# Kernel optimization log

Hardware: AMD Instinct MI355X
Metric: run time of the kernel (lower is better)

## Reference

```python
import jax, jax.numpy as jnp
import numpy as np

N = 8192   # num_nodes
H = 128    # hidden_dim
B = 100    # batch of events
K = 5      # num_neg_samples
TD_MAX = 10000.0
TIME_SD = jnp.array([50.0, 7.0, 15.0, 15.0])  # time_sd from forward; time_mean = 0


def setup_inputs() -> dict:
    key = jax.random.key(0)
    ks = jax.random.split(key, 16)
    p = 32.0 / N  # avg degree ~32
    A = (jax.random.uniform(ks[0], (N, N)) < p).astype(jnp.float32)
    # S init: S[v,u] = 1/D[v] for neighbors u (row-normalized A)
    S = A / (A.sum(axis=1, keepdims=True) + 1e-7)
    z0 = jax.random.normal(ks[1], (N, H)) * 0.1
    u = jax.random.randint(ks[2], (B,), 0, N)
    v = jax.random.randint(ks[3], (B,), 0, N)
    event_types = jax.random.randint(ks[4], (B,), 0, 2)
    neg_idx = jax.random.randint(ks[5], (B, 2 * K), 0, N)
    time_diff = jax.random.normal(ks[6], (B, 2, 4))
    t_bar = jax.random.uniform(ks[7], (B, N)) * 1000.0
    t = 1000.0 + 10.0 * jnp.arange(B, dtype=jnp.float32)

    def lin(k, o, i):
        k1, k2 = jax.random.split(k)
        lim = 1.0 / np.sqrt(i)
        return (jax.random.uniform(k1, (o, i), minval=-lim, maxval=lim),
                jax.random.uniform(k2, (o,), minval=-lim, maxval=lim))

    om0_w, om0_b = lin(ks[8], 1, 2 * H)
    om1_w, om1_b = lin(ks[9], 1, 2 * H)
    Wh_w, Wh_b = lin(ks[10], H, H)
    Ws_w, Ws_b = lin(ks[11], H, H)
    Wr_w, Wr_b = lin(ks[12], H, H)
    Wt_w, Wt_b = lin(ks[13], H, 4)
    return dict(u=u, v=v, event_types=event_types, neg_idx=neg_idx,
                time_diff=time_diff, t_bar=t_bar, t=t, z0=z0, A=A, S=S,
                w_t=0.5 * jnp.ones(2), alpha=0.5 * jnp.ones(2), psi=0.5 * jnp.ones(2),
                om0_w=om0_w, om0_b=om0_b, om1_w=om1_w, om1_b=om1_b,
                Wh_w=Wh_w, Wh_b=Wh_b, Ws_w=Ws_w, Ws_b=Ws_b,
                Wr_w=Wr_w, Wr_b=Wr_b, Wt_w=Wt_w, Wt_b=Wt_b)


def _forward(u, v, event_types, neg_idx, time_diff, t_bar, t, z0, A, S,
             w_t, alpha, psi, om0_w, om0_b, om1_w, om1_b,
             Wh_w, Wh_b, Ws_w, Ws_b, Wr_w, Wr_b, Wt_w, Wt_b):
    td_norm = time_diff / TIME_SD  # (td - 0) / sd

    def hawkes(zu, zv, et, td):
        # lambda = psi * log(1 + exp(g/psi)) + alpha * exp(-w_t * td/td_max)
        zc = jnp.concatenate([zu, zv], axis=-1)
        g0 = jnp.einsum('...d,d->...', zc, om0_w[0]) + om0_b[0]
        g1 = jnp.einsum('...d,d->...', zc, om1_w[0]) + om1_b[0]
        g = jnp.where(et == 0, g0, g1)
        ps, al, wt = psi[et], alpha[et], w_t[et]
        gp = jnp.clip(g / (ps + 1e-7), -75.0, 75.0)
        return ps * jnp.log1p(jnp.exp(gp)) + al * jnp.exp(-wt * (td / TD_MAX))

    ar = jnp.arange(N)

    def step(z, ev):
        u_it, v_it, et, td2, tb, t_it, neg = ev
        z_u, z_v = z[u_it], z[v_it]
        Wh_all = z @ Wh_w.T + Wh_b  # [N,H]

        def struct(node):
            # structural attention over node's neighbors (masked, not dense loop)
            mask = A[node] > 0
            q = jnp.exp(S[node]) * mask
            q = q / (q.sum() + 1e-7)
            hsig = jax.nn.sigmoid(q[:, None] * Wh_all)
            hmax = jnp.where(mask[:, None], hsig, -jnp.inf).max(axis=0)
            return jnp.where(jnp.any(mask), hmax, 0.0)

        # update of u uses struct info from v's neighborhood, and vice versa
        hs = jnp.stack([struct(v_it), struct(u_it)])  # [2,H]
        h = (hs @ Ws_w.T + Ws_b) + (jnp.stack([z_u, z_v]) @ Wr_w.T + Wr_b) + (td2 @ Wt_w.T + Wt_b)
        z_upd = jax.nn.sigmoid(h)
        z_new = z.at[u_it].set(z_upd[0]).at[v_it].set(z_upd[1])

        # negative pairs: (u, v_neg_k) then (u_neg_k, v), using z_prev
        v_neg, u_neg = neg[:K], neg[K:]
        zu_neg = jnp.concatenate([jnp.broadcast_to(z_u, (K, H)), z[u_neg]], 0)
        zv_neg = jnp.concatenate([z[v_neg], jnp.broadcast_to(z_v, (K, H))], 0)
        lt_u = jnp.concatenate([jnp.full((K,), tb[u_it]), tb[u_neg]])
        lt_v = jnp.concatenate([tb[v_neg], jnp.full((K,), tb[v_it])])
        ts_neg = t_it - jnp.maximum(lt_u, lt_v)
        ts_pos = t_it - jnp.maximum(tb[u_it], tb[v_it])

        # all-node intensity prediction (Lambda_dict path, detached in torch)
        zd = jax.lax.stop_gradient(z)
        zu_all = jnp.concatenate([jnp.broadcast_to(jax.lax.stop_gradient(z_u), (N, H)),
                                  jnp.broadcast_to(jax.lax.stop_gradient(z_v), (N, H))], 0)
        zv_all = jnp.concatenate([zd, zd], 0)
        last_t = jnp.maximum(
            jnp.concatenate([jnp.full((N,), tb[u_it]), jnp.full((N,), tb[v_it])]),
            jnp.concatenate([tb, tb]))
        lam_all = hawkes(zu_all, zv_all, jnp.full((2 * N,), et),
                         jax.lax.stop_gradient(t_it - last_t))
        m = ((ar != u_it) & (ar != v_it)).astype(lam_all.dtype)
        lam_sum = jax.lax.stop_gradient(jnp.sum(lam_all * jnp.concatenate([m, m])))

        return z_new, (z_u, z_v, zu_neg, zv_neg, ts_pos, ts_neg, lam_sum)

    _, (zu_p, zv_p, zun, zvn, ts_p, ts_n, lam_sums) = jax.lax.scan(
        step, z0, (u, v, event_types, td_norm, t_bar, t, neg_idx))

    lam_pos = hawkes(zu_p, zv_p, event_types, ts_p)            # [B]
    lam_neg = hawkes(zun, zvn, event_types[:, None], ts_n)      # [B,2K]
    return jnp.concatenate([lam_pos[:, None], lam_neg, lam_sums[:, None]], axis=1)  # [B, 2K+2]


def reference(u, v, event_types, neg_idx, time_diff, t_bar, t, z0, A, S,
              w_t, alpha, psi, om0_w, om0_b, om1_w, om1_b,
              Wh_w, Wh_b, Ws_w, Ws_b, Wr_w, Wr_b, Wt_w, Wt_b):
    return _forward(u, v, event_types, neg_idx, time_diff, t_bar, t, z0, A, S,
                    w_t, alpha, psi, om0_w, om0_b, om1_w, om1_b,
                    Wh_w, Wh_b, Ws_w, Ws_b, Wr_w, Wr_b, Wt_w, Wt_b)
```

## Files before the change

kernel.cpp:

```cpp
#include <hip/hip_runtime.h>
#include <math.h>

#define N 8192
#define H 128
#define BB 100
#define KK 5
#define MAXN 256
#define TD_MAXF 10000.0f

#define OFF_WHALLV ((size_t)N * H)
#define OFF_ZVER (OFF_WHALLV + 2 * BB * H)

__global__ __launch_bounds__(256) void prep_weights_kernel(
    const float* __restrict__ Wh, const float* __restrict__ Ws,
    const float* __restrict__ Wr, const float* __restrict__ om0,
    const float* __restrict__ om1, float* __restrict__ WhT,
    float* __restrict__ WsT, float* __restrict__ WrT, float* __restrict__ omP,
    unsigned* __restrict__ flags) {
  int idx = blockIdx.x * 256 + threadIdx.x;
  if (idx < H * H) {
    int d = idx >> 7, k = idx & (H - 1);
    WhT[k * H + d] = Wh[d * H + k];
  } else if (idx < 2 * H * H) {
    int e = idx - H * H;
    int d = e >> 7, k = e & (H - 1);
    WsT[k * H + d] = Ws[d * H + k];
  } else if (idx < 3 * H * H) {
    int e = idx - 2 * H * H;
    int d = e >> 7, k = e & (H - 1);
    WrT[k * H + d] = Wr[d * H + k];
  } else if (idx < 3 * H * H + 2 * H) {
    int e = idx - 3 * H * H;
    omP[e] = om0[e];
  } else if (idx < 3 * H * H + 4 * H) {
    int e = idx - 3 * H * H - 2 * H;
    omP[2 * H + e] = om1[e];
  } else if (idx < 3 * H * H + 4 * H + 4 * BB + 4) {
    int e = idx - (3 * H * H + 4 * H);
    flags[e] = 0u;
  }
}

__global__ __launch_bounds__(256) void dbase_kernel(
    const float* __restrict__ z0, const float* __restrict__ om0,
    const float* __restrict__ om1, float* __restrict__ dvec0) {
  int j = blockIdx.x * 256 + threadIdx.x;
  if (j >= N) return;
  const float4* zr = (const float4*)(z0 + (size_t)j * H);
  const float4* o0 = (const float4*)om0;
  const float4* o1 = (const float4*)om1;
  float a0 = 0, b0 = 0, a1 = 0, b1 = 0;
  for (int k = 0; k < H / 4; ++k) {
    float4 zv = zr[k];
    float4 l0 = o0[k], r0 = o0[k + H / 4];
    float4 l1 = o1[k], r1 = o1[k + H / 4];
    a0 += zv.x * l0.x + zv.y * l0.y + zv.z * l0.z + zv.w * l0.w;
    b0 += zv.x * r0.x + zv.y * r0.y + zv.z * r0.z + zv.w * r0.w;
    a1 += zv.x * l1.x + zv.y * l1.y + zv.z * l1.z + zv.w * l1.w;
    b1 += zv.x * r1.x + zv.y * r1.y + zv.z * r1.z + zv.w * r1.w;
  }
  dvec0[0 * N + j] = a0;
  dvec0[1 * N + j] = b0;
  dvec0[2 * N + j] = a1;
  dvec0[3 * N + j] = b1;
}

__global__ __launch_bounds__(128) void whall_kernel(
    const float* __restrict__ z0, const float* __restrict__ WhT,
    const float* __restrict__ Wh_b, float* __restrict__ whall) {
  int n = blockIdx.x;
  __shared__ float zr[H];
  zr[threadIdx.x] = z0[(size_t)n * H + threadIdx.x];
  __syncthreads();
  int d = threadIdx.x;
  float acc = Wh_b[d];
#pragma unroll 8
  for (int k = 0; k < H; ++k) acc += zr[k] * WhT[k * H + d];
  whall[(size_t)n * H + d] = acc;
}

__global__ __launch_bounds__(256) void nbr_kernel(
    const int* __restrict__ u, const int* __restrict__ v,
    const float* __restrict__ A, const float* __restrict__ S,
    int* __restrict__ cnt, int* __restrict__ nidx, float* __restrict__ nes,
    float* __restrict__ qsum) {
  int l = blockIdx.x;
  int b = l >> 1, r = l & 1;
  int node = r ? u[b] : v[b];
  const int tid = threadIdx.x;
  __shared__ int cnts[256];
  __shared__ int excl[257];
  __shared__ float ssum[256];
  int c = 0;
  float local = 0.0f;
  for (int it = 0; it < N / 256; ++it) {
    int j = it * 256 + tid;
    if (A[(size_t)node * N + j] > 0.0f) {
      ++c;
      local += expf(S[(size_t)node * N + j]);
    }
  }
  cnts[tid] = c;
  ssum[tid] = local;
  __syncthreads();
  if (tid == 0) {
    int s = 0;
    for (int i = 0; i < 256; ++i) { excl[i] = s; s += cnts[i]; }
    excl[256] = s;
  }
  __syncthreads();
  int p = excl[tid];
  for (int it = 0; it < N / 256; ++it) {
    int j = it * 256 + tid;
    if (A[(size_t)node * N + j] > 0.0f) {
      if (p < MAXN) {
        nidx[l * MAXN + p] = j;
        nes[l * MAXN + p] = expf(S[(size_t)node * N + j]);
      }
      ++p;
    }
  }
  __syncthreads();
  for (int s = 128; s > 0; s >>= 1) {
    if (tid < s) ssum[tid] += ssum[tid + s];
    __syncthreads();
  }
  if (tid == 0) {
    cnt[l] = min(excl[256], MAXN);
    qsum[l] = ssum[0];
  }
}

__global__ __launch_bounds__(256) void dag_prep_kernel(
    const int* __restrict__ u_, const int* __restrict__ v_,
    const int* __restrict__ cnt_, const int* __restrict__ nidx_,
    int* __restrict__ woff, int* __restrict__ zsrc, unsigned* __restrict__ need) {
  int l = blockIdx.x;
  int b = l >> 1, r = l & 1;
  const int tid = threadIdx.x;
  __shared__ int uL[BB], vL[BB];
  if (tid < BB) {
    uL[tid] = u_[tid];
    vL[tid] = v_[tid];
  }
  __syncthreads();
  int c = cnt_[l];
  for (int i = tid; i < c; i += 256) {
    int n = nidx_[l * MAXN + i];
    int a = -1, row = 0;
    for (int s = b - 1; s >= 0; --s) {
      if (vL[s] == n) { a = s; row = 1; break; }
      if (uL[s] == n) { a = s; row = 0; break; }
    }
    int off;
    if (a < 0) {
      off = n * H;
    } else {
      off = (int)OFF_WHALLV + (2 * a + row) * H;
      atomicOr(&need[b * 4 + (a >> 5)], 1u << (a & 31));
    }
    woff[l * MAXN + i] = off;
  }
  if (r == 0 && tid >= 254) {
    int which = tid - 254;
    int node = which ? vL[b] : uL[b];
    int a = -1, row = 0;
    for (int s = b - 1; s >= 0; --s) {
      if (vL[s] == node) { a = s; row = 1; break; }
      if (uL[s] == node) { a = s; row = 0; break; }
    }
    int sv = -1;
    if (a >= 0) {
      sv = 2 * a + row;
      atomicOr(&need[b * 4 + (a >> 5)], 1u << (a & 31));
    }
    zsrc[2 * b + which] = sv;
  }
}

__global__ __launch_bounds__(1024) void step_kernel(
    const int* __restrict__ u_, const int* __restrict__ v_,
    const float* __restrict__ time_diff, const float* __restrict__ z0,
    const float* __restrict__ WhT, const float* __restrict__ WsT,
    const float* __restrict__ WrT, const float* __restrict__ omP,
    const float* __restrict__ Wh_b, const float* __restrict__ Ws_b,
    const float* __restrict__ Wr_b, const float* __restrict__ Wt_w,
    const float* __restrict__ Wt_b, const float* __restrict__ wsf,
    float* __restrict__ zver, float* __restrict__ whallv,
    float* __restrict__ dlog, const float* __restrict__ qsum_,
    const int* __restrict__ cnt_, const float* __restrict__ nes_,
    const int* __restrict__ woff_, const int* __restrict__ zsrc_,
    const unsigned* __restrict__ need, unsigned* done) {
  const int b = blockIdx.x;
  const int t = threadIdx.x;
  __shared__ int woffS[2][MAXN];
  __shared__ float nqS[2][MAXN];
  __shared__ float scratch[8][2][H];
  __shared__ float hsS[2][H];
  __shared__ float zrowS[2][H];
  __shared__ float zupdS[2][H];
  __shared__ float td2S[2][4];
  __shared__ int cntS[2], zsrcS[2], uvS[2];
  __shared__ float invqS[2];

  if (t < 512) {
    int r = t >> 8, i = t & 255;
    int l = 2 * b + r;
    woffS[r][i] = woff_[l * MAXN + i];
    nqS[r][i] = nes_[l * MAXN + i];
  } else if (t < 520) {
    int i = t - 512;
    int c = i & 3;
    float sd = (c == 0) ? 50.0f : ((c == 1) ? 7.0f : 15.0f);
    td2S[i >> 2][c] = time_diff[b * 8 + i] / sd;
  } else if (t < 522) {
    int r = t - 520;
    cntS[r] = cnt_[2 * b + r];
    invqS[r] = 1.0f / (qsum_[2 * b + r] + 1e-7f);
    zsrcS[r] = zsrc_[2 * b + r];
  } else if (t == 522) {
    uvS[0] = u_[b];
  } else if (t == 523) {
    uvS[1] = v_[b];
  }
  if (t == 0) {
    for (int w = 0; w < 4; ++w) {
      unsigned nw = need[b * 4 + w];
      while ((atomicOr(&done[w], 0u) & nw) != nw) __builtin_amdgcn_s_sleep(1);
    }
    __threadfence();
  }
  __syncthreads();

  const int ub = uvS[0], vb = uvS[1];

  {
    int r = t >> 9;
    int sub = (t >> 7) & 3;
    int d = t & (H - 1);
    int c = cntS[r];
    float iq = invqS[r];
    float mx = -INFINITY;
#pragma unroll 4
    for (int i = sub; i < c; i += 4)
      mx = fmaxf(mx, nqS[r][i] * iq * wsf[(size_t)woffS[r][i] + d]);
    scratch[sub][r][d] = mx;
  }
  if (t < 256) {
    int r = t >> 7, d = t & (H - 1);
    int s = zsrcS[r];
    int node = r ? vb : ub;
    if (s < 0)
      zrowS[r][d] = z0[(size_t)node * H + d];
    else
      zrowS[r][d] = wsf[OFF_ZVER + (size_t)s * H + d];
  }
  __syncthreads();

  if (t < 2 * H) {
    int r = t >> 7, d = t & (H - 1);
    float m = fmaxf(fmaxf(scratch[0][r][d], scratch[1][r][d]),
                    fmaxf(scratch[2][r][d], scratch[3][r][d]));
    hsS[r][d] = (cntS[r] > 0) ? (1.0f / (1.0f + expf(-m))) : 0.0f;
  }
  __syncthreads();

  {
    int ks = t >> 7;
    int d = t & (H - 1);
    int k0 = ks * 16;
    float a0 = 0.0f, a1 = 0.0f;
#pragma unroll 4
    for (int k = k0; k < k0 + 16; ++k) {
      float ws = WsT[k * H + d], wr = WrT[k * H + d];
      a0 += hsS[0][k] * ws + zrowS[0][k] * wr;
      a1 += hsS[1][k] * ws + zrowS[1][k] * wr;
    }
    scratch[ks][0][d] = a0;
    scratch[ks][1][d] = a1;
  }
  __syncthreads();

  if (t < 2 * H) {
    int r = t >> 7, d = t & (H - 1);
    float acc = Ws_b[d] + Wr_b[d] + Wt_b[d];
#pragma unroll
    for (int ks = 0; ks < 8; ++ks) acc += scratch[ks][r][d];
    acc += td2S[r][0] * Wt_w[d * 4 + 0] + td2S[r][1] * Wt_w[d * 4 + 1] +
           td2S[r][2] * Wt_w[d * 4 + 2] + td2S[r][3] * Wt_w[d * 4 + 3];
    float zu = 1.0f / (1.0f + expf(-acc));
    zupdS[r][d] = zu;
    zver[(size_t)(2 * b + r) * H + d] = zu;
  }
  __syncthreads();

  {
    int ks = t >> 7;
    int d = t & (H - 1);
    int k0 = ks * 16;
    int r0 = (ub == vb) ? 1 : 0;
    float a0 = 0.0f, a1 = 0.0f;
#pragma unroll 4
    for (int k = k0; k < k0 + 16; ++k) {
      float wh = WhT[k * H + d];
      a0 += zupdS[r0][k] * wh;
      a1 += zupdS[1][k] * wh;
    }
    scratch[ks][0][d] = a0;
    scratch[ks][1][d] = a1;
  }
  __syncthreads();

  if (t < 2 * H) {
    int r = t >> 7, d = t & (H - 1);
    float acc = Wh_b[d];
#pragma unroll
    for (int ks = 0; ks < 8; ++ks) acc += scratch[ks][r][d];
    whallv[(size_t)(2 * b + r) * H + d] = acc;
  } else if (t < 768) {
    int w = (t - 256) >> 6;
    int lane = t & 63;
    int row = w >> 2;
    int which = w & 3;
    int rr = (row == 0 && ub == vb) ? 1 : row;
    int wsel = which >> 1;
    int off = (which & 1) * H;
    float val = zupdS[rr][lane] * omP[wsel * 2 * H + off + lane] +
                zupdS[rr][64 + lane] * omP[wsel * 2 * H + off + 64 + lane];
    for (int s = 32; s > 0; s >>= 1) val += __shfl_down(val, s);
    if (lane == 0) dlog[b * 8 + which * 2 + row] = val;
  }
  __syncthreads();

  if (t == 0) {
    __threadfence();
    atomicOr(&done[b >> 5], 1u << (b & 31));
  }
}

__global__ __launch_bounds__(256) void lam_kernel(
    const int* __restrict__ u, const int* __restrict__ v,
    const int* __restrict__ etypes, const int* __restrict__ neg_,
    const float* __restrict__ t_bar, const float* __restrict__ tt,
    const float* __restrict__ w_t, const float* __restrict__ alpha,
    const float* __restrict__ psi, const float* __restrict__ om0_b,
    const float* __restrict__ om1_b, const float* __restrict__ dvec0,
    const float* __restrict__ dlog, float* __restrict__ out) {
  const int b = blockIdx.x;
  const int tid = threadIdx.x;
  __shared__ float dR[N];
  __shared__ int uS[BB], vS[BB];
  __shared__ float red[256];
  __shared__ float suS, svS;

  const int e = etypes[b];
  const int ub = u[b], vb = v[b];
  const float ps = psi[e], al = alpha[e], wt = w_t[e];
  const float ob0 = om0_b[0], ob1 = om1_b[0];
  const float ob = e ? ob1 : ob0;
  const float tcur = tt[b];
  const float inv_ps = 1.0f / (ps + 1e-7f);
  const int whichR = 2 * e + 1;
  const int whichL = 2 * e;

  if (tid < BB) {
    uS[tid] = u[tid];
    vS[tid] = v[tid];
  }
  {
    const float4* base = (const float4*)(dvec0 + (size_t)whichR * N);
    float4* dst = (float4*)dR;
    for (int i = tid; i < N / 4; i += 256) dst[i] = base[i];
  }
  __syncthreads();

  for (int i = tid; i < b; i += 256) {
    int ui = uS[i], vi = vS[i];
    bool u_over = (ui == vi);
    bool v_over = false;
    for (int j = i + 1; j < b; ++j) {
      int uj = uS[j], vj = vS[j];
      u_over = u_over || (uj == ui) || (vj == ui);
      v_over = v_over || (uj == vi) || (vj == vi);
    }
    if (!u_over) dR[ui] = dlog[i * 8 + whichR * 2 + 0];
    if (!v_over) dR[vi] = dlog[i * 8 + whichR * 2 + 1];
  }

  if (tid < 13) {
    auto dpre = [&](int x, int which) -> float {
      for (int bp = b - 1; bp >= 0; --bp) {
        if (vS[bp] == x) return dlog[bp * 8 + which * 2 + 1];
        if (uS[bp] == x) return dlog[bp * 8 + which * 2 + 0];
      }
      return dvec0[(size_t)which * N + x];
    };
    if (tid < 11) {
      int li, ri;
      float ltu, ltv;
      if (tid == 0) {
        li = ub; ri = vb;
        ltu = t_bar[(size_t)b * N + ub];
        ltv = t_bar[(size_t)b * N + vb];
      } else if (tid <= 5) {
        int vn = neg_[b * (2 * KK) + (tid - 1)];
        li = ub; ri = vn;
        ltu = t_bar[(size_t)b * N + ub];
        ltv = t_bar[(size_t)b * N + vn];
      } else {
        int un = neg_[b * (2 * KK) + (tid - 1)];
        li = un; ri = vb;
        ltu = t_bar[(size_t)b * N + un];
        ltv = t_bar[(size_t)b * N + vb];
      }
      float g = dpre(li, whichL) + dpre(ri, whichR) + ob;
      float gp = fminf(fmaxf(g * inv_ps, -75.0f), 75.0f);
      float ts = tcur - fmaxf(ltu, ltv);
      out[b * 12 + tid] =
          ps * log1pf(expf(gp)) + al * expf(-wt * (ts / TD_MAXF));
    } else if (tid == 11) {
      suS = dpre(ub, whichL);
    } else {
      svS = dpre(vb, whichL);
    }
  }
  __syncthreads();

  const float su = suS, sv = svS;
  const float tb_u = t_bar[(size_t)b * N + ub];
  const float tb_v = t_bar[(size_t)b * N + vb];
  float acc = 0.0f;
  for (int j = tid; j < N; j += 256) {
    if (j == ub || j == vb) continue;
    float d = dR[j];
    float tbj = t_bar[(size_t)b * N + j];
    float gu = su + d + ob;
    float gv = sv + d + ob;
    float gpu_ = fminf(fmaxf(gu * inv_ps, -75.0f), 75.0f);
    float gpv_ = fminf(fmaxf(gv * inv_ps, -75.0f), 75.0f);
    float spl = ps * (log1pf(expf(gpu_)) + log1pf(expf(gpv_)));
    float tdu = tcur - fmaxf(tb_u, tbj);
    float tdv = tcur - fmaxf(tb_v, tbj);
    float ex = al * (expf(-wt * (tdu / TD_MAXF)) + expf(-wt * (tdv / TD_MAXF)));
    acc += spl + ex;
  }
  red[tid] = acc;
  __syncthreads();
  for (int s = 128; s > 0; s >>= 1) {
    if (tid < s) red[tid] += red[tid + s];
    __syncthreads();
  }
  if (tid == 0) out[b * 12 + 11] = red[0];
}

extern "C" void kernel_launch(void* const* d_in, const int* in_sizes, int n_in,
                              void* d_out, int out_size, void* d_ws,
                              size_t ws_size, hipStream_t stream) {
  const int* u = (const int*)d_in[0];
  const int* v = (const int*)d_in[1];
  const int* et = (const int*)d_in[2];
  const int* neg = (const int*)d_in[3];
  const float* time_diff = (const float*)d_in[4];
  const float* t_bar = (const float*)d_in[5];
  const float* t = (const float*)d_in[6];
  const float* z0 = (const float*)d_in[7];
  const float* A = (const float*)d_in[8];
  const float* S = (const float*)d_in[9];
  const float* w_t = (const float*)d_in[10];
  const float* alpha = (const float*)d_in[11];
  const float* psi = (const float*)d_in[12];
  const float* om0_w = (const float*)d_in[13];
  const float* om0_b = (const float*)d_in[14];
  const float* om1_w = (const float*)d_in[15];
  const float* om1_b = (const float*)d_in[16];
  const float* Wh_w = (const float*)d_in[17];
  const float* Wh_b = (const float*)d_in[18];
  const float* Ws_w = (const float*)d_in[19];
  const float* Ws_b = (const float*)d_in[20];
  const float* Wr_w = (const float*)d_in[21];
  const float* Wr_b = (const float*)d_in[22];
  const float* Wt_w = (const float*)d_in[23];
  const float* Wt_b = (const float*)d_in[24];
  float* out = (float*)d_out;

  float* wsf = (float*)d_ws;
  float* whall = wsf;
  float* whallv = wsf + OFF_WHALLV;
  float* zver = wsf + OFF_ZVER;
  float* WhT = zver + 2 * BB * H;
  float* WsT = WhT + H * H;
  float* WrT = WsT + H * H;
  float* omP = WrT + H * H;
  float* dvec0 = omP + 4 * H;
  float* dlog = dvec0 + 4 * N;
  float* qsum = dlog + 8 * BB;
  int* cnt = (int*)(qsum + 2 * BB);
  int* nidx = cnt + 2 * BB;
  float* nes = (float*)(nidx + 2 * BB * MAXN);
  int* woff = (int*)(nes + 2 * BB * MAXN);
  int* zsrc = woff + 2 * BB * MAXN;
  unsigned* need = (unsigned*)(zsrc + 2 * BB);
  unsigned* done = need + 4 * BB;

  prep_weights_kernel<<<(3 * H * H + 4 * H + 4 * BB + 4 + 255) / 256, 256, 0,
                        stream>>>(Wh_w, Ws_w, Wr_w, om0_w, om1_w, WhT, WsT,
                                  WrT, omP, need);
  dbase_kernel<<<(N + 255) / 256, 256, 0, stream>>>(z0, om0_w, om1_w, dvec0);
  whall_kernel<<<N, H, 0, stream>>>(z0, WhT, Wh_b, whall);
  nbr_kernel<<<2 * BB, 256, 0, stream>>>(u, v, A, S, cnt, nidx, nes, qsum);
  dag_prep_kernel<<<2 * BB, 256, 0, stream>>>(u, v, cnt, nidx, woff, zsrc,
                                              need);
  step_kernel<<<BB, 1024, 0, stream>>>(
      u, v, time_diff, z0, WhT, WsT, WrT, omP, Wh_b, Ws_b, Wr_b, Wt_w, Wt_b,
      wsf, zver, whallv, dlog, qsum, cnt, nes, woff, zsrc, need, done);
  lam_kernel<<<BB, 256, 0, stream>>>(u, v, et, neg, t_bar, t, w_t, alpha, psi,
                                     om0_b, om1_b, dvec0, dlog, out);
}
```

Baseline: 645.9 us.

## Merge prep kernels, prefetch independent neighbors before dependency wait, widen lam kernel

```diff
diff --git a/kernel.cpp b/kernel.cpp
--- a/kernel.cpp
+++ b/kernel.cpp
@@ -11,86 +11,89 @@
 #define OFF_WHALLV ((size_t)N * H)
 #define OFF_ZVER (OFF_WHALLV + 2 * BB * H)
 
-__global__ __launch_bounds__(256) void prep_weights_kernel(
+__global__ __launch_bounds__(256) void prep_all_kernel(
     const float* __restrict__ Wh, const float* __restrict__ Ws,
     const float* __restrict__ Wr, const float* __restrict__ om0,
-    const float* __restrict__ om1, float* __restrict__ WhT,
-    float* __restrict__ WsT, float* __restrict__ WrT, float* __restrict__ omP,
-    unsigned* __restrict__ flags) {
+    const float* __restrict__ om1, const float* __restrict__ z0,
+    float* __restrict__ WhT, float* __restrict__ WsT, float* __restrict__ WrT,
+    float* __restrict__ omP, unsigned* __restrict__ flags,
+    float* __restrict__ dvec0) {
+  const int B0 = H * H, B1 = 2 * H * H, B2 = 3 * H * H;
+  const int B3 = B2 + 2 * H, B4 = B2 + 4 * H, B5 = B4 + 4 * BB + 4;
   int idx = blockIdx.x * 256 + threadIdx.x;
-  if (idx < H * H) {
+  if (idx < B0) {
     int d = idx >> 7, k = idx & (H - 1);
     WhT[k * H + d] = Wh[d * H + k];
-  } else if (idx < 2 * H * H) {
-    int e = idx - H * H;
+  } else if (idx < B1) {
+    int e = idx - B0;
     int d = e >> 7, k = e & (H - 1);
     WsT[k * H + d] = Ws[d * H + k];
-  } else if (idx < 3 * H * H) {
-    int e = idx - 2 * H * H;
+  } else if (idx < B2) {
+    int e = idx - B1;
     int d = e >> 7, k = e & (H - 1);
     WrT[k * H + d] = Wr[d * H + k];
-  } else if (idx < 3 * H * H + 2 * H) {
-    int e = idx - 3 * H * H;
+  } else if (idx < B3) {
+    int e = idx - B2;
     omP[e] = om0[e];
-  } else if (idx < 3 * H * H + 4 * H) {
-    int e = idx - 3 * H * H - 2 * H;
+  } else if (idx < B4) {
+    int e = idx - B3;
     omP[2 * H + e] = om1[e];
-  } else if (idx < 3 * H * H + 4 * H + 4 * BB + 4) {
-    int e = idx - (3 * H * H + 4 * H);
-    flags[e] = 0u;
+  } else if (idx < B5) {
+    flags[idx - B4] = 0u;
+  } else if (idx < B5 + N) {
+    int j = idx - B5;
+    const float4* zr = (const float4*)(z0 + (size_t)j * H);
+    const float4* o0 = (const float4*)om0;
+    const float4* o1 = (const float4*)om1;
+    float a0 = 0, b0 = 0, a1 = 0, b1 = 0;
+    for (int k = 0; k < H / 4; ++k) {
+      float4 zv = zr[k];
+      float4 l0 = o0[k], r0 = o0[k + H / 4];
+      float4 l1 = o1[k], r1 = o1[k + H / 4];
+      a0 += zv.x * l0.x + zv.y * l0.y + zv.z * l0.z + zv.w * l0.w;
+      b0 += zv.x * r0.x + zv.y * r0.y + zv.z * r0.z + zv.w * r0.w;
+      a1 += zv.x * l1.x + zv.y * l1.y + zv.z * l1.z + zv.w * l1.w;
+      b1 += zv.x * r1.x + zv.y * r1.y + zv.z * r1.z + zv.w * r1.w;
+    }
+    dvec0[0 * N + j] = a0;
+    dvec0[1 * N + j] = b0;
+    dvec0[2 * N + j] = a1;
+    dvec0[3 * N + j] = b1;
   }
 }
 
-__global__ __launch_bounds__(256) void dbase_kernel(
-    const float* __restrict__ z0, const float* __restrict__ om0,
-    const float* __restrict__ om1, float* __restrict__ dvec0) {
-  int j = blockIdx.x * 256 + threadIdx.x;
-  if (j >= N) return;
-  const float4* zr = (const float4*)(z0 + (size_t)j * H);
-  const float4* o0 = (const float4*)om0;
-  const float4* o1 = (const float4*)om1;
-  float a0 = 0, b0 = 0, a1 = 0, b1 = 0;
-  for (int k = 0; k < H / 4; ++k) {
-    float4 zv = zr[k];
-    float4 l0 = o0[k], r0 = o0[k + H / 4];
-    float4 l1 = o1[k], r1 = o1[k + H / 4];
-    a0 += zv.x * l0.x + zv.y * l0.y + zv.z * l0.z + zv.w * l0.w;
-    b0 += zv.x * r0.x + zv.y * r0.y + zv.z * r0.z + zv.w * r0.w;
-    a1 += zv.x * l1.x + zv.y * l1.y + zv.z * l1.z + zv.w * l1.w;
-    b1 += zv.x * r1.x + zv.y * r1.y + zv.z * r1.z + zv.w * r1.w;
-  }
-  dvec0[0 * N + j] = a0;
-  dvec0[1 * N + j] = b0;
-  dvec0[2 * N + j] = a1;
-  dvec0[3 * N + j] = b1;
-}
-
-__global__ __launch_bounds__(128) void whall_kernel(
+__global__ __launch_bounds__(256) void build_kernel(
     const float* __restrict__ z0, const float* __restrict__ WhT,
-    const float* __restrict__ Wh_b, float* __restrict__ whall) {
-  int n = blockIdx.x;
-  __shared__ float zr[H];
-  zr[threadIdx.x] = z0[(size_t)n * H + threadIdx.x];
-  __syncthreads();
-  int d = threadIdx.x;
-  float acc = Wh_b[d];
-#pragma unroll 8
-  for (int k = 0; k < H; ++k) acc += zr[k] * WhT[k * H + d];
-  whall[(size_t)n * H + d] = acc;
-}
-
-__global__ __launch_bounds__(256) void nbr_kernel(
-    const int* __restrict__ u, const int* __restrict__ v,
+    const float* __restrict__ Wh_b, float* __restrict__ whall,
+    const int* __restrict__ u_, const int* __restrict__ v_,
     const float* __restrict__ A, const float* __restrict__ S,
     int* __restrict__ cnt, int* __restrict__ nidx, float* __restrict__ nes,
-    float* __restrict__ qsum) {
-  int l = blockIdx.x;
-  int b = l >> 1, r = l & 1;
-  int node = r ? u[b] : v[b];
+    float* __restrict__ qsum, int* __restrict__ woff, int* __restrict__ zsrc,
+    unsigned* __restrict__ need) {
+  const int blk = blockIdx.x;
   const int tid = threadIdx.x;
+  __shared__ float zr2[2][H];
   __shared__ int cnts[256];
   __shared__ int excl[257];
   __shared__ float ssum[256];
+  __shared__ int nidxL[MAXN];
+  __shared__ int uL[BB], vL[BB];
+
+  if (blk < N / 2) {
+    int r = tid >> 7, d = tid & (H - 1);
+    int row = blk * 2 + r;
+    zr2[r][d] = z0[(size_t)row * H + d];
+    __syncthreads();
+    float acc = Wh_b[d];
+#pragma unroll 8
+    for (int k = 0; k < H; ++k) acc += zr2[r][k] * WhT[k * H + d];
+    whall[(size_t)row * H + d] = acc;
+    return;
+  }
+
+  const int l = blk - N / 2;
+  const int b = l >> 1, r = l & 1;
+  const int node = r ? u_[b] : v_[b];
   int c = 0;
   float local = 0.0f;
   for (int it = 0; it < N / 256; ++it) {
@@ -115,38 +118,28 @@
     if (A[(size_t)node * N + j] > 0.0f) {
       if (p < MAXN) {
         nidx[l * MAXN + p] = j;
+        nidxL[p] = j;
         nes[l * MAXN + p] = expf(S[(size_t)node * N + j]);
       }
       ++p;
     }
   }
+  if (tid < BB) {
+    uL[tid] = u_[tid];
+    vL[tid] = v_[tid];
+  }
   __syncthreads();
   for (int s = 128; s > 0; s >>= 1) {
     if (tid < s) ssum[tid] += ssum[tid + s];
     __syncthreads();
   }
+  const int cM = min(excl[256], MAXN);
   if (tid == 0) {
-    cnt[l] = min(excl[256], MAXN);
+    cnt[l] = cM;
     qsum[l] = ssum[0];
   }
-}
-
-__global__ __launch_bounds__(256) void dag_prep_kernel(
-    const int* __restrict__ u_, const int* __restrict__ v_,
-    const int* __restrict__ cnt_, const int* __restrict__ nidx_,
-    int* __restrict__ woff, int* __restrict__ zsrc, unsigned* __restrict__ need) {
-  int l = blockIdx.x;
-  int b = l >> 1, r = l & 1;
-  const int tid = threadIdx.x;
-  __shared__ int uL[BB], vL[BB];
-  if (tid < BB) {
-    uL[tid] = u_[tid];
-    vL[tid] = v_[tid];
-  }
-  __syncthreads();
-  int c = cnt_[l];
-  for (int i = tid; i < c; i += 256) {
-    int n = nidx_[l * MAXN + i];
+  for (int i = tid; i < cM; i += 256) {
+    int n = nidxL[i];
     int a = -1, row = 0;
     for (int s = b - 1; s >= 0; --s) {
       if (vL[s] == n) { a = s; row = 1; break; }
@@ -163,11 +156,11 @@
   }
   if (r == 0 && tid >= 254) {
     int which = tid - 254;
-    int node = which ? vL[b] : uL[b];
+    int nd = which ? vL[b] : uL[b];
     int a = -1, row = 0;
     for (int s = b - 1; s >= 0; --s) {
-      if (vL[s] == node) { a = s; row = 1; break; }
-      if (uL[s] == node) { a = s; row = 0; break; }
+      if (vL[s] == nd) { a = s; row = 1; break; }
+      if (uL[s] == nd) { a = s; row = 0; break; }
     }
     int sv = -1;
     if (a >= 0) {
@@ -193,40 +186,52 @@
     const unsigned* __restrict__ need, unsigned* done) {
   const int b = blockIdx.x;
   const int t = threadIdx.x;
-  __shared__ int woffS[2][MAXN];
-  __shared__ float nqS[2][MAXN];
   __shared__ float scratch[8][2][H];
   __shared__ float hsS[2][H];
   __shared__ float zrowS[2][H];
   __shared__ float zupdS[2][H];
   __shared__ float td2S[2][4];
-  __shared__ int cntS[2], zsrcS[2], uvS[2];
-  __shared__ float invqS[2];
-
-  if (t < 512) {
-    int r = t >> 8, i = t & 255;
-    int l = 2 * b + r;
-    woffS[r][i] = woff_[l * MAXN + i];
-    nqS[r][i] = nes_[l * MAXN + i];
-  } else if (t < 520) {
+  __shared__ int uvS[2];
+
+  const int r = t >> 9;
+  const int sub = (t >> 7) & 3;
+  const int d = t & (H - 1);
+  const int l = 2 * b + r;
+  const int c = cnt_[l];
+  const float iq = 1.0f / (qsum_[l] + 1e-7f);
+
+  float mx = -INFINITY;
+  for (int i = sub; i < c; i += 4) {
+    int off = woff_[l * MAXN + i];
+    if (off < (int)OFF_WHALLV)
+      mx = fmaxf(mx, nes_[l * MAXN + i] * iq * wsf[(size_t)off + d]);
+  }
+  float zpre = 0.0f;
+  int zs = -1;
+  if (t < 256) {
+    int rr = t >> 7, dd = t & (H - 1);
+    zs = zsrc_[2 * b + rr];
+    if (zs < 0) {
+      int nd = rr ? v_[b] : u_[b];
+      zpre = z0[(size_t)nd * H + dd];
+    }
+  }
+  if (t >= 512 && t < 520) {
     int i = t - 512;
-    int c = i & 3;
-    float sd = (c == 0) ? 50.0f : ((c == 1) ? 7.0f : 15.0f);
-    td2S[i >> 2][c] = time_diff[b * 8 + i] / sd;
-  } else if (t < 522) {
-    int r = t - 520;
-    cntS[r] = cnt_[2 * b + r];
-    invqS[r] = 1.0f / (qsum_[2 * b + r] + 1e-7f);
-    zsrcS[r] = zsrc_[2 * b + r];
-  } else if (t == 522) {
+    int cc = i & 3;
+    float sd = (cc == 0) ? 50.0f : ((cc == 1) ? 7.0f : 15.0f);
+    td2S[i >> 2][cc] = time_diff[b * 8 + i] / sd;
+  }
+  if (t == 0) {
     uvS[0] = u_[b];
-  } else if (t == 523) {
     uvS[1] = v_[b];
-  }
-  if (t == 0) {
     for (int w = 0; w < 4; ++w) {
       unsigned nw = need[b * 4 + w];
-      while ((atomicOr(&done[w], 0u) & nw) != nw) __builtin_amdgcn_s_sleep(1);
+      if (!nw) continue;
+      while ((__hip_atomic_load(&done[w], __ATOMIC_RELAXED,
+                                __HIP_MEMORY_SCOPE_AGENT) &
+              nw) != nw)
+        __builtin_amdgcn_s_sleep(1);
     }
     __threadfence();
   }
@@ -234,40 +239,37 @@
 
   const int ub = uvS[0], vb = uvS[1];
 
-  {
-    int r = t >> 9;
-    int sub = (t >> 7) & 3;
-    int d = t & (H - 1);
-    int c = cntS[r];
-    float iq = invqS[r];
-    float mx = -INFINITY;
-#pragma unroll 4
-    for (int i = sub; i < c; i += 4)
-      mx = fmaxf(mx, nqS[r][i] * iq * wsf[(size_t)woffS[r][i] + d]);
-    scratch[sub][r][d] = mx;
-  }
+  for (int i = sub; i < c; i += 4) {
+    int off = woff_[l * MAXN + i];
+    if (off >= (int)OFF_WHALLV)
+      mx = fmaxf(mx, nes_[l * MAXN + i] * iq * wsf[(size_t)off + d]);
+  }
+  scratch[sub][r][d] = mx;
   if (t < 256) {
-    int r = t >> 7, d = t & (H - 1);
-    int s = zsrcS[r];
-    int node = r ? vb : ub;
-    if (s < 0)
-      zrowS[r][d] = z0[(size_t)node * H + d];
+    int rr = t >> 7, dd = t & (H - 1);
+    float zv;
+    if (zs < 0)
+      zv = zpre;
     else
-      zrowS[r][d] = wsf[OFF_ZVER + (size_t)s * H + d];
+      zv = wsf[OFF_ZVER + (size_t)zs * H + dd];
+    zrowS[rr][dd] = zv;
   }
   __syncthreads();
 
   if (t < 2 * H) {
-    int r = t >> 7, d = t & (H - 1);
-    float m = fmaxf(fmaxf(scratch[0][r][d], scratch[1][r][d]),
-                    fmaxf(scratch[2][r][d], scratch[3][r][d]));
-    hsS[r][d] = (cntS[r] > 0) ? (1.0f / (1.0f + expf(-m))) : 0.0f;
+    int rr = t >> 7, dd = t & (H - 1);
+    float m = fmaxf(fmaxf(scratch[0][rr][dd], scratch[1][rr][dd]),
+                    fmaxf(scratch[2][rr][dd], scratch[3][rr][dd]));
+    hsS[rr][dd] = (c > 0 || rr != r || true)
+                      ? ((cnt_[2 * b + rr] > 0)
+                             ? (1.0f / (1.0f + expf(-m)))
+                             : 0.0f)
+                      : 0.0f;
   }
   __syncthreads();
 
   {
     int ks = t >> 7;
-    int d = t & (H - 1);
     int k0 = ks * 16;
     float a0 = 0.0f, a1 = 0.0f;
 #pragma unroll 4
@@ -282,21 +284,20 @@
   __syncthreads();
 
   if (t < 2 * H) {
-    int r = t >> 7, d = t & (H - 1);
-    float acc = Ws_b[d] + Wr_b[d] + Wt_b[d];
+    int rr = t >> 7, dd = t & (H - 1);
+    float acc = Ws_b[dd] + Wr_b[dd] + Wt_b[dd];
 #pragma unroll
-    for (int ks = 0; ks < 8; ++ks) acc += scratch[ks][r][d];
-    acc += td2S[r][0] * Wt_w[d * 4 + 0] + td2S[r][1] * Wt_w[d * 4 + 1] +
-           td2S[r][2] * Wt_w[d * 4 + 2] + td2S[r][3] * Wt_w[d * 4 + 3];
+    for (int ks = 0; ks < 8; ++ks) acc += scratch[ks][rr][dd];
+    acc += td2S[rr][0] * Wt_w[dd * 4 + 0] + td2S[rr][1] * Wt_w[dd * 4 + 1] +
+           td2S[rr][2] * Wt_w[dd * 4 + 2] + td2S[rr][3] * Wt_w[dd * 4 + 3];
     float zu = 1.0f / (1.0f + expf(-acc));
-    zupdS[r][d] = zu;
-    zver[(size_t)(2 * b + r) * H + d] = zu;
+    zupdS[rr][dd] = zu;
+    zver[(size_t)(2 * b + rr) * H + dd] = zu;
   }
   __syncthreads();
 
   {
     int ks = t >> 7;
-    int d = t & (H - 1);
     int k0 = ks * 16;
     int r0 = (ub == vb) ? 1 : 0;
     float a0 = 0.0f, a1 = 0.0f;
@@ -312,11 +313,11 @@
   __syncthreads();
 
   if (t < 2 * H) {
-    int r = t >> 7, d = t & (H - 1);
-    float acc = Wh_b[d];
+    int rr = t >> 7, dd = t & (H - 1);
+    float acc = Wh_b[dd];
 #pragma unroll
-    for (int ks = 0; ks < 8; ++ks) acc += scratch[ks][r][d];
-    whallv[(size_t)(2 * b + r) * H + d] = acc;
+    for (int ks = 0; ks < 8; ++ks) acc += scratch[ks][rr][dd];
+    whallv[(size_t)(2 * b + rr) * H + dd] = acc;
   } else if (t < 768) {
     int w = (t - 256) >> 6;
     int lane = t & 63;
@@ -338,7 +339,7 @@
   }
 }
 
-__global__ __launch_bounds__(256) void lam_kernel(
+__global__ __launch_bounds__(1024) void lam_kernel(
     const int* __restrict__ u, const int* __restrict__ v,
     const int* __restrict__ etypes, const int* __restrict__ neg_,
     const float* __restrict__ t_bar, const float* __restrict__ tt,
@@ -350,7 +351,7 @@
   const int tid = threadIdx.x;
   __shared__ float dR[N];
   __shared__ int uS[BB], vS[BB];
-  __shared__ float red[256];
+  __shared__ float red[1024];
   __shared__ float suS, svS;
 
   const int e = etypes[b];
@@ -370,11 +371,11 @@
   {
     const float4* base = (const float4*)(dvec0 + (size_t)whichR * N);
     float4* dst = (float4*)dR;
-    for (int i = tid; i < N / 4; i += 256) dst[i] = base[i];
-  }
-  __syncthreads();
-
-  for (int i = tid; i < b; i += 256) {
+    for (int i = tid; i < N / 4; i += 1024) dst[i] = base[i];
+  }
+  __syncthreads();
+
+  for (int i = tid; i < b; i += 1024) {
     int ui = uS[i], vi = vS[i];
     bool u_over = (ui == vi);
     bool v_over = false;
@@ -429,24 +430,35 @@
   const float su = suS, sv = svS;
   const float tb_u = t_bar[(size_t)b * N + ub];
   const float tb_v = t_bar[(size_t)b * N + vb];
+  const float4* tb4 = (const float4*)(t_bar + (size_t)b * N);
+  const float4* dR4 = (const float4*)dR;
   float acc = 0.0f;
-  for (int j = tid; j < N; j += 256) {
-    if (j == ub || j == vb) continue;
-    float d = dR[j];
-    float tbj = t_bar[(size_t)b * N + j];
-    float gu = su + d + ob;
-    float gv = sv + d + ob;
-    float gpu_ = fminf(fmaxf(gu * inv_ps, -75.0f), 75.0f);
-    float gpv_ = fminf(fmaxf(gv * inv_ps, -75.0f), 75.0f);
-    float spl = ps * (log1pf(expf(gpu_)) + log1pf(expf(gpv_)));
-    float tdu = tcur - fmaxf(tb_u, tbj);
-    float tdv = tcur - fmaxf(tb_v, tbj);
-    float ex = al * (expf(-wt * (tdu / TD_MAXF)) + expf(-wt * (tdv / TD_MAXF)));
-    acc += spl + ex;
+  for (int j4 = tid; j4 < N / 4; j4 += 1024) {
+    float4 dv = dR4[j4];
+    float4 tb = tb4[j4];
+    float de[4] = {dv.x, dv.y, dv.z, dv.w};
+    float te[4] = {tb.x, tb.y, tb.z, tb.w};
+#pragma unroll
+    for (int ee = 0; ee < 4; ++ee) {
+      int j = j4 * 4 + ee;
+      if (j == ub || j == vb) continue;
+      float dd = de[ee];
+      float tbj = te[ee];
+      float gu = su + dd + ob;
+      float gv = sv + dd + ob;
+      float gpu_ = fminf(fmaxf(gu * inv_ps, -75.0f), 75.0f);
+      float gpv_ = fminf(fmaxf(gv * inv_ps, -75.0f), 75.0f);
+      float spl = ps * (log1pf(expf(gpu_)) + log1pf(expf(gpv_)));
+      float tdu = tcur - fmaxf(tb_u, tbj);
+      float tdv = tcur - fmaxf(tb_v, tbj);
+      float ex =
+          al * (expf(-wt * (tdu / TD_MAXF)) + expf(-wt * (tdv / TD_MAXF)));
+      acc += spl + ex;
+    }
   }
   red[tid] = acc;
   __syncthreads();
-  for (int s = 128; s > 0; s >>= 1) {
+  for (int s = 512; s > 0; s >>= 1) {
     if (tid < s) red[tid] += red[tid + s];
     __syncthreads();
   }
@@ -502,17 +514,15 @@
   unsigned* need = (unsigned*)(zsrc + 2 * BB);
   unsigned* done = need + 4 * BB;
 
-  prep_weights_kernel<<<(3 * H * H + 4 * H + 4 * BB + 4 + 255) / 256, 256, 0,
-                        stream>>>(Wh_w, Ws_w, Wr_w, om0_w, om1_w, WhT, WsT,
-                                  WrT, omP, need);
-  dbase_kernel<<<(N + 255) / 256, 256, 0, stream>>>(z0, om0_w, om1_w, dvec0);
-  whall_kernel<<<N, H, 0, stream>>>(z0, WhT, Wh_b, whall);
-  nbr_kernel<<<2 * BB, 256, 0, stream>>>(u, v, A, S, cnt, nidx, nes, qsum);
-  dag_prep_kernel<<<2 * BB, 256, 0, stream>>>(u, v, cnt, nidx, woff, zsrc,
-                                              need);
+  const int PREP_ELEMS = 3 * H * H + 4 * H + 4 * BB + 4 + N;
+  prep_all_kernel<<<(PREP_ELEMS + 255) / 256, 256, 0, stream>>>(
+      Wh_w, Ws_w, Wr_w, om0_w, om1_w, z0, WhT, WsT, WrT, omP, need, dvec0);
+  build_kernel<<<N / 2 + 2 * BB, 256, 0, stream>>>(
+      z0, WhT, Wh_b, whall, u, v, A, S, cnt, nidx, nes, qsum, woff, zsrc,
+      need);
   step_kernel<<<BB, 1024, 0, stream>>>(
       u, v, time_diff, z0, WhT, WsT, WrT, omP, Wh_b, Ws_b, Wr_b, Wt_w, Wt_b,
       wsf, zver, whallv, dlog, qsum, cnt, nes, woff, zsrc, need, done);
-  lam_kernel<<<BB, 256, 0, stream>>>(u, v, et, neg, t_bar, t, w_t, alpha, psi,
-                                     om0_b, om1_b, dvec0, dlog, out);
+  lam_kernel<<<BB, 1024, 0, stream>>>(u, v, et, neg, t_bar, t, w_t, alpha, psi,
+                                      om0_b, om1_b, dvec0, dlog, out);
 }
```

After: 610.3 us. 5.5% less time.
